# Optimization experiments

Measured on AMD Instinct MI355X. Metric: run time of the kernel, lower is better.

The kernel has to match this reference:

```python
import jax, jax.numpy as jnp
import numpy as np

# Static problem sizes (uniform T/taus make the ragged edge list static).
B, N, F, T, TAU, S = 8, 384, 64, 192, 192, 5
SINK_SHIFT = T                    # min sink index == T (sinks are the new nodes)
N_SINK, N_SOURCE = TAU, T + TAU - 1


def _edge_indices():
    # tril_indices(T+tau, offset=-1), keep sink >= T  (window=None)
    r, c = np.tril_indices(T + TAU, k=-1)
    m = r >= T
    r, c = r[m], c[m]
    e = r.shape[0]
    batch = np.repeat(np.arange(B), e)
    return (jnp.asarray(batch, jnp.int32),
            jnp.asarray(np.tile(r, B), jnp.int32),
            jnp.asarray(np.tile(c, B), jnp.int32))


def setup_inputs() -> dict:
    key = jax.random.key(0)
    ks = jax.random.split(key, 6)
    batch_idx, sink_idx, source_idx = _edge_indices()
    s1, s2 = 1.0 / np.sqrt(2 * F), 1.0 / np.sqrt(F)
    return {
        "nodes": jax.random.normal(ks[0], (B, N, F), jnp.float32),
        "w1": jax.random.uniform(ks[1], (2 * F, F), jnp.float32, -s1, s1),
        "b1": jnp.zeros((F,), jnp.float32),
        "g1": jnp.ones((F,), jnp.float32),
        "be1": jnp.zeros((F,), jnp.float32),
        "w2": jax.random.uniform(ks[2], (F, F), jnp.float32, -s2, s2),
        "b2": jnp.zeros((F,), jnp.float32),
        "g2": jnp.ones((F,), jnp.float32),
        "be2": jnp.zeros((F,), jnp.float32),
        "w3": jax.random.uniform(ks[3], (F, 1), jnp.float32, -s2, s2),
        "b3": jnp.zeros((1,), jnp.float32),
        "gumbel": jax.random.gumbel(ks[4], (S, B, N_SINK, N_SOURCE), jnp.float32),
        "batch_idx": batch_idx,
        "sink_idx": sink_idx,
        "source_idx": source_idx,
    }


def _ln(x, g, b):
    mu = x.mean(-1, keepdims=True)
    v = ((x - mu) ** 2).mean(-1, keepdims=True)
    return (x - mu) * jax.lax.rsqrt(v + 1e-5) * g + b


def reference(nodes, w1, b1, g1, be1, w2, b2, g2, be2, w3, b3,
              gumbel, batch_idx, sink_idx, source_idx):
    # gather sink/source node pairs: [E, 2F]
    sink = nodes[batch_idx, sink_idx]
    src = nodes[batch_idx, source_idx]
    x = jnp.concatenate([sink, src], axis=-1)
    # edge MLP -> per-edge logit
    h = _ln(jax.nn.relu(x @ w1 + b1), g1, be1)
    h = _ln(jax.nn.relu(h @ w2 + b2), g2, be2)
    logits = (h @ w3 + b3)[:, 0]                     # [E]
    # dense-padded grid filled with finfo.min (as in torch)
    neg = jnp.finfo(jnp.float32).min
    gs = jnp.full((B, N_SINK, N_SOURCE), neg, jnp.float32)
    gs = gs.at[batch_idx, sink_idx - SINK_SHIFT, source_idx].set(logits)
    # hard gumbel-softmax over source dim, S independent samples
    y_soft = jax.nn.softmax(gs[None] + gumbel, axis=-1)      # [S,B,192,383]
    y_hard = jax.nn.one_hot(jnp.argmax(y_soft, -1), N_SOURCE, dtype=y_soft.dtype)
    y = y_soft + jax.lax.stop_gradient(y_hard - y_soft)
    e = y.sum(0)
    # straight-through binarize: forward (e>0), backward identity
    e = e + jax.lax.stop_gradient((e > 0).astype(e.dtype) - e)
    valid = e[batch_idx, sink_idx - SINK_SHIFT, source_idx]
    vals = jnp.where(valid > 0, valid, 0.0)
    # dense equivalent of the sparse COO adjacency (B, N, N)
    return jnp.zeros((B, N, N), jnp.float32).at[batch_idx, sink_idx, source_idx].set(vals)
```

## Files before the change

kernel.cpp:

```cpp
#include <hip/hip_runtime.h>
#include <math.h>
#include <stdint.h>

#define BB 8
#define NN 384
#define FF 64
#define TT 192
#define NSRC 383
#define NSINK 192
#define SS 5
#define NEDGE 441600
#define BN (BB * NN)
#define TILE_E 256
#define NBLKE (NEDGE / TILE_E)
#define OUTV ((BB * NN * NN) / 4)

typedef _Float16 half8 __attribute__((ext_vector_type(8)));
typedef __fp16 fp16x2 __attribute__((ext_vector_type(2)));
typedef float floatx4 __attribute__((ext_vector_type(4)));

static __device__ __forceinline__ void split_f16(float x, uint16_t& h, uint16_t& l) {
  const _Float16 hh = (_Float16)x;
  const float hb = (float)hh;
  const _Float16 ll = (_Float16)((x - hb) * 512.f);
  h = __builtin_bit_cast(uint16_t, hh);
  l = __builtin_bit_cast(uint16_t, ll);
}

static __device__ __forceinline__ void split_pair(float x0, float x1,
                                                  uint32_t& hi, uint32_t& lo) {
  const fp16x2 h = __builtin_amdgcn_cvt_pkrtz(x0, x1);
  const float hb0 = (float)h.x, hb1 = (float)h.y;
  const fp16x2 l = __builtin_amdgcn_cvt_pkrtz((x0 - hb0) * 512.f, (x1 - hb1) * 512.f);
  hi = __builtin_bit_cast(uint32_t, h);
  lo = __builtin_bit_cast(uint32_t, l);
}

__global__ __launch_bounds__(64) void prep_all(
    const float* __restrict__ nodes, const float* __restrict__ w1,
    const float* __restrict__ b1,
    const float* __restrict__ w2, const float* __restrict__ b2,
    const float* __restrict__ g1, const float* __restrict__ be1,
    const float* __restrict__ g2, const float* __restrict__ be2,
    const float* __restrict__ w3, const float* __restrict__ b3,
    float* __restrict__ A, float* __restrict__ Bv,
    unsigned short* __restrict__ Whg, unsigned short* __restrict__ Wlg,
    float* __restrict__ wcol, float* __restrict__ cb,
    float* __restrict__ gw, float* __restrict__ cwsgw) {
  const int blk = blockIdx.x;
  const int k = threadIdx.x;
  if (blk < BN / 4) {
    const int bn0 = blk * 4;
    __shared__ float nd[4][FF];
#pragma unroll
    for (int i = 0; i < 4; ++i) nd[i][k] = nodes[(bn0 + i) * FF + k];
    __syncthreads();
    const float bk = b1[k];
    float a0 = bk, a1 = bk, a2 = bk, a3 = bk;
    float q0 = 0.f, q1 = 0.f, q2 = 0.f, q3 = 0.f;
#pragma unroll 8
    for (int f = 0; f < FF; ++f) {
      const float wt = w1[f * FF + k];
      const float wb = w1[(FF + f) * FF + k];
      const float n0 = nd[0][f], n1 = nd[1][f], n2 = nd[2][f], n3 = nd[3][f];
      a0 = fmaf(n0, wt, a0); a1 = fmaf(n1, wt, a1);
      a2 = fmaf(n2, wt, a2); a3 = fmaf(n3, wt, a3);
      q0 = fmaf(n0, wb, q0); q1 = fmaf(n1, wb, q1);
      q2 = fmaf(n2, wb, q2); q3 = fmaf(n3, wb, q3);
    }
    A[(bn0 + 0) * FF + k] = a0;  Bv[(bn0 + 0) * FF + k] = q0;
    A[(bn0 + 1) * FF + k] = a1;  Bv[(bn0 + 1) * FF + k] = q1;
    A[(bn0 + 2) * FF + k] = a2;  Bv[(bn0 + 2) * FF + k] = q2;
    A[(bn0 + 3) * FF + k] = a3;  Bv[(bn0 + 3) * FF + k] = q3;
  } else {
    const int j = k;
    const int jt = j >> 4, m = j & 15;
    float cbj = b2[j];
    float wc = 0.f;
    for (int kk = 0; kk < FF; ++kk) {
      const float wraw = w2[kk * FF + j];
      const float w = g1[kk] * wraw;
      wc += w;
      cbj = fmaf(be1[kk], wraw, cbj);
      uint16_t hu, lu;
      split_f16(w, hu, lu);
      const int kc = kk >> 5, qq = (kk >> 3) & 3, jj = kk & 7;
      const int idx = (((jt * 2 + kc) * 4 + qq) * 16 + m) * 8 + jj;
      Whg[idx] = hu;
      Wlg[idx] = lu;
    }
    wcol[j] = wc;
    cb[j] = cbj;
    const float gwj = g2[j] * w3[j];
    gw[j] = gwj;
    __shared__ float sA[FF], sB[FF];
    sA[j] = gwj;
    sB[j] = be2[j] * w3[j];
    __syncthreads();
    if (j == 0) {
      float a = 0.f, bq = 0.f;
      for (int i = 0; i < FF; ++i) { a += sA[i]; bq += sB[i]; }
      cwsgw[0] = b3[0] + bq;
      cwsgw[1] = a;
    }
  }
}

__global__ __launch_bounds__(256, 2) void edge_mlp(
    const float* __restrict__ A, const float* __restrict__ Bv,
    const unsigned short* __restrict__ Whg, const unsigned short* __restrict__ Wlg,
    const float* __restrict__ wcolg, const float* __restrict__ cbg,
    const float* __restrict__ gwg, const float* __restrict__ cwsgw,
    const int* __restrict__ bidx, const int* __restrict__ ridx,
    const int* __restrict__ cidx, float* __restrict__ L,
    float4* __restrict__ outv) {
  __shared__ __align__(16) unsigned short XHs[16384];
  __shared__ __align__(16) unsigned short XLs[16384];

  const int tid = threadIdx.x;
  const int wave = tid >> 6;
  const int lane = tid & 63;
  const int q4 = lane >> 4;
  const int c15 = lane & 15;

  const int gtid = blockIdx.x * 256 + tid;
  if (gtid < OUTV) outv[gtid] = make_float4(0.f, 0.f, 0.f, 0.f);

  half8 whr[4][2], wlr[4][2];
#pragma unroll
  for (int jt = 0; jt < 4; ++jt)
#pragma unroll
    for (int kc = 0; kc < 2; ++kc) {
      const int woff = ((jt * 2 + kc) * 4 + q4) * 128 + c15 * 8;
      whr[jt][kc] = *(const half8*)&Whg[woff];
      wlr[jt][kc] = *(const half8*)&Wlg[woff];
    }

  const int ge = blockIdx.x * TILE_E + tid;
  const int b = bidx[ge], r = ridx[ge], c = cidx[ge];
  const int et_own = lane >> 4, n_own = lane & 15;
  float mu, rstd;
  {
    const float4* pa = (const float4*)(A + (b * NN + r) * FF);
    const float4* pb = (const float4*)(Bv + (b * NN + c) * FF);
    unsigned short* dh = &XHs[wave * 4096 + n_own * 8];
    unsigned short* dl = &XLs[wave * 4096 + n_own * 8];
    float s = 0.f, q = 0.f;
#pragma unroll
    for (int g = 0; g < 8; ++g) {
      const float4 av0 = pa[2 * g], av1 = pa[2 * g + 1];
      const float4 bv0 = pb[2 * g], bv1 = pb[2 * g + 1];
      const float x0 = fmaxf(av0.x + bv0.x, 0.f);
      const float x1 = fmaxf(av0.y + bv0.y, 0.f);
      const float x2 = fmaxf(av0.z + bv0.z, 0.f);
      const float x3 = fmaxf(av0.w + bv0.w, 0.f);
      const float x4 = fmaxf(av1.x + bv1.x, 0.f);
      const float x5 = fmaxf(av1.y + bv1.y, 0.f);
      const float x6 = fmaxf(av1.z + bv1.z, 0.f);
      const float x7 = fmaxf(av1.w + bv1.w, 0.f);
      s += x0 + x1 + x2 + x3 + x4 + x5 + x6 + x7;
      q = fmaf(x0, x0, q); q = fmaf(x1, x1, q);
      q = fmaf(x2, x2, q); q = fmaf(x3, x3, q);
      q = fmaf(x4, x4, q); q = fmaf(x5, x5, q);
      q = fmaf(x6, x6, q); q = fmaf(x7, x7, q);
      int4 hi4, lo4;
      split_pair(x0, x1, *(uint32_t*)&hi4.x, *(uint32_t*)&lo4.x);
      split_pair(x2, x3, *(uint32_t*)&hi4.y, *(uint32_t*)&lo4.y);
      split_pair(x4, x5, *(uint32_t*)&hi4.z, *(uint32_t*)&lo4.z);
      split_pair(x6, x7, *(uint32_t*)&hi4.w, *(uint32_t*)&lo4.w);
      const int choff = ((et_own * 2 + (g >> 2)) * 4 + (g & 3)) * 128;
      *(int4*)(dh + choff) = hi4;
      *(int4*)(dl + choff) = lo4;
    }
    mu = s * (1.f / FF);
    rstd = 1.f / sqrtf(q * (1.f / FF) - mu * mu + 1e-5f);
  }

  __syncthreads();

  floatx4 wc4[4], cb4[4], gw4[4];
#pragma unroll
  for (int jt = 0; jt < 4; ++jt) {
    wc4[jt] = *(const floatx4*)(wcolg + 16 * jt + 4 * q4);
    cb4[jt] = *(const floatx4*)(cbg + 16 * jt + 4 * q4);
    gw4[jt] = *(const floatx4*)(gwg + 16 * jt + 4 * q4);
  }
  const float cw = cwsgw[0], sgw = cwsgw[1];

#pragma unroll
  for (int et = 0; et < 4; ++et) {
    floatx4 acc0[4], acc1[4];
#pragma unroll
    for (int jt = 0; jt < 4; ++jt) {
      acc0[jt] = (floatx4){0.f, 0.f, 0.f, 0.f};
      acc1[jt] = (floatx4){0.f, 0.f, 0.f, 0.f};
    }
#pragma unroll
    for (int kc = 0; kc < 2; ++kc) {
      const int xoff = wave * 4096 + ((et * 2 + kc) * 4 + q4) * 128 + c15 * 8;
      const half8 xh = *(const half8*)&XHs[xoff];
      const half8 xl = *(const half8*)&XLs[xoff];
#pragma unroll
      for (int jt = 0; jt < 4; ++jt) {
        acc0[jt] = __builtin_amdgcn_mfma_f32_16x16x32_f16(whr[jt][kc], xh, acc0[jt], 0, 0, 0);
        acc1[jt] = __builtin_amdgcn_mfma_f32_16x16x32_f16(whr[jt][kc], xl, acc1[jt], 0, 0, 0);
        acc1[jt] = __builtin_amdgcn_mfma_f32_16x16x32_f16(wlr[jt][kc], xh, acc1[jt], 0, 0, 0);
      }
    }
    const int e2 = 16 * et + c15;
    const float mue = __shfl(mu, e2, 64);
    const float rse = __shfl(rstd, e2, 64);
    float s1 = 0.f, s2 = 0.f, s3 = 0.f;
#pragma unroll
    for (int jt = 0; jt < 4; ++jt) {
      const floatx4 t4 = acc0[jt] + acc1[jt] * (1.f / 512.f);
#pragma unroll
      for (int rg = 0; rg < 4; ++rg) {
        const float pre = fmaf(rse, fmaf(-mue, wc4[jt][rg], t4[rg]), cb4[jt][rg]);
        const float tr = fmaxf(pre, 0.f);
        s1 += tr;
        s2 = fmaf(tr, tr, s2);
        s3 = fmaf(tr, gw4[jt][rg], s3);
      }
    }
    s1 += __shfl_xor(s1, 16, 64); s1 += __shfl_xor(s1, 32, 64);
    s2 += __shfl_xor(s2, 16, 64); s2 += __shfl_xor(s2, 32, 64);
    s3 += __shfl_xor(s3, 16, 64); s3 += __shfl_xor(s3, 32, 64);
    const int b2 = __shfl(b, e2, 64);
    const int r2 = __shfl(r, e2, 64);
    const int c2 = __shfl(c, e2, 64);
    if (q4 == 0) {
      const float mu2 = s1 * (1.f / FF);
      const float var2 = s2 * (1.f / FF) - mu2 * mu2;
      const float rstd2 = 1.f / sqrtf(var2 + 1e-5f);
      const float logit = fmaf(rstd2, fmaf(-mu2, sgw, s3), cw);
      L[(b2 * NSINK + (r2 - TT)) * NSRC + c2] = logit;
    }
  }
}

__global__ __launch_bounds__(256) void argmax_scatter(
    const float* __restrict__ L, const float* __restrict__ gum,
    float* __restrict__ out) {
  const int task = blockIdx.x * 4 + (threadIdx.x >> 6);
  const int lane = threadIdx.x & 63;
  const int row = task % NSINK;
  const int sb = task / NSINK;
  const int b = sb & 7;
  const int r = row + TT;

  const float* __restrict__ lrow = L + (b * NSINK + row) * NSRC;
  const float* __restrict__ grow = gum + task * NSRC;

  float bv = -INFINITY;
  int bi = 0;
  for (int c = lane; c < r; c += 64) {
    const float v = lrow[c] + grow[c];
    if (v > bv) { bv = v; bi = c; }
  }
#pragma unroll
  for (int off = 32; off > 0; off >>= 1) {
    const float ov = __shfl_xor(bv, off, 64);
    const int oi = __shfl_xor(bi, off, 64);
    if (ov > bv || (ov == bv && oi < bi)) { bv = ov; bi = oi; }
  }
  if (lane == 0) out[(b * NN + r) * NN + bi] = 1.0f;
}

extern "C" void kernel_launch(void* const* d_in, const int* in_sizes, int n_in,
                              void* d_out, int out_size, void* d_ws, size_t ws_size,
                              hipStream_t stream) {
  const float* nodes = (const float*)d_in[0];
  const float* w1 = (const float*)d_in[1];
  const float* b1 = (const float*)d_in[2];
  const float* g1 = (const float*)d_in[3];
  const float* be1 = (const float*)d_in[4];
  const float* w2 = (const float*)d_in[5];
  const float* b2 = (const float*)d_in[6];
  const float* g2 = (const float*)d_in[7];
  const float* be2 = (const float*)d_in[8];
  const float* w3 = (const float*)d_in[9];
  const float* b3 = (const float*)d_in[10];
  const float* gum = (const float*)d_in[11];
  const int* bidx = (const int*)d_in[12];
  const int* ridx = (const int*)d_in[13];
  const int* cidx = (const int*)d_in[14];
  float* out = (float*)d_out;

  float* ws = (float*)d_ws;
  float* A = ws;
  float* Bv = A + BN * FF;
  unsigned short* Whg = (unsigned short*)(ws + 393216);
  unsigned short* Wlg = Whg + 4096;
  float* wcol = ws + 397312;
  float* cb = wcol + FF;
  float* gw = cb + FF;
  float* cwsgw = gw + FF;
  float* L = ws + 397520;
  (void)ws_size; (void)n_in; (void)in_sizes; (void)out_size;

  hipLaunchKernelGGL(prep_all, dim3(BN / 4 + 1), dim3(64), 0, stream,
                     nodes, w1, b1, w2, b2, g1, be1, g2, be2, w3, b3,
                     A, Bv, Whg, Wlg, wcol, cb, gw, cwsgw);
  hipLaunchKernelGGL(edge_mlp, dim3(NBLKE), dim3(256), 0, stream,
                     A, Bv, Whg, Wlg, wcol, cb, gw, cwsgw, bidx, ridx, cidx, L,
                     (float4*)out);
  hipLaunchKernelGGL(argmax_scatter, dim3((SS * BB * NSINK) / 4), dim3(256), 0, stream,
                     L, gum, out);
}
```

Before: 132.9 us.

## Transpose B projection layout, defer weight loads, merge samples in argmax

The source-side projection Bv is stored feature-chunk-major, so adjacent edges (consecutive source columns) read adjacent float4s and the gather coalesces. The MFMA weight register loads move after the gather phase, and a __syncthreads is removed. argmax_scatter now handles all 5 gumbel samples in one wave per (batch,row), reading each logit once and cutting the wave count fivefold. The risks are less parallelism in argmax, higher register pressure, and a possible LDS race from the removed barrier if waves share XHs regions.

```diff
diff --git a/kernel.cpp b/kernel.cpp
--- a/kernel.cpp
+++ b/kernel.cpp
@@ -68,10 +68,15 @@
       q0 = fmaf(n0, wb, q0); q1 = fmaf(n1, wb, q1);
       q2 = fmaf(n2, wb, q2); q3 = fmaf(n3, wb, q3);
     }
-    A[(bn0 + 0) * FF + k] = a0;  Bv[(bn0 + 0) * FF + k] = q0;
-    A[(bn0 + 1) * FF + k] = a1;  Bv[(bn0 + 1) * FF + k] = q1;
-    A[(bn0 + 2) * FF + k] = a2;  Bv[(bn0 + 2) * FF + k] = q2;
-    A[(bn0 + 3) * FF + k] = a3;  Bv[(bn0 + 3) * FF + k] = q3;
+    A[(bn0 + 0) * FF + k] = a0;
+    A[(bn0 + 1) * FF + k] = a1;
+    A[(bn0 + 2) * FF + k] = a2;
+    A[(bn0 + 3) * FF + k] = a3;
+    const int f4 = k >> 2, ff = k & 3;
+    Bv[(f4 * BN + (bn0 + 0)) * 4 + ff] = q0;
+    Bv[(f4 * BN + (bn0 + 1)) * 4 + ff] = q1;
+    Bv[(f4 * BN + (bn0 + 2)) * 4 + ff] = q2;
+    Bv[(f4 * BN + (bn0 + 3)) * 4 + ff] = q3;
   } else {
     const int j = k;
     const int jt = j >> 4, m = j & 15;
@@ -126,30 +131,22 @@
   const int gtid = blockIdx.x * 256 + tid;
   if (gtid < OUTV) outv[gtid] = make_float4(0.f, 0.f, 0.f, 0.f);
 
-  half8 whr[4][2], wlr[4][2];
-#pragma unroll
-  for (int jt = 0; jt < 4; ++jt)
-#pragma unroll
-    for (int kc = 0; kc < 2; ++kc) {
-      const int woff = ((jt * 2 + kc) * 4 + q4) * 128 + c15 * 8;
-      whr[jt][kc] = *(const half8*)&Whg[woff];
-      wlr[jt][kc] = *(const half8*)&Wlg[woff];
-    }
-
   const int ge = blockIdx.x * TILE_E + tid;
   const int b = bidx[ge], r = ridx[ge], c = cidx[ge];
   const int et_own = lane >> 4, n_own = lane & 15;
   float mu, rstd;
   {
     const float4* pa = (const float4*)(A + (b * NN + r) * FF);
-    const float4* pb = (const float4*)(Bv + (b * NN + c) * FF);
+    const float4* pb4 = (const float4*)Bv;
+    const int colB = b * NN + c;
     unsigned short* dh = &XHs[wave * 4096 + n_own * 8];
     unsigned short* dl = &XLs[wave * 4096 + n_own * 8];
     float s = 0.f, q = 0.f;
 #pragma unroll
     for (int g = 0; g < 8; ++g) {
       const float4 av0 = pa[2 * g], av1 = pa[2 * g + 1];
-      const float4 bv0 = pb[2 * g], bv1 = pb[2 * g + 1];
+      const float4 bv0 = pb4[(2 * g) * BN + colB];
+      const float4 bv1 = pb4[(2 * g + 1) * BN + colB];
       const float x0 = fmaxf(av0.x + bv0.x, 0.f);
       const float x1 = fmaxf(av0.y + bv0.y, 0.f);
       const float x2 = fmaxf(av0.z + bv0.z, 0.f);
@@ -176,7 +173,15 @@
     rstd = 1.f / sqrtf(q * (1.f / FF) - mu * mu + 1e-5f);
   }
 
-  __syncthreads();
+  half8 whr[4][2], wlr[4][2];
+#pragma unroll
+  for (int jt = 0; jt < 4; ++jt)
+#pragma unroll
+    for (int kc = 0; kc < 2; ++kc) {
+      const int woff = ((jt * 2 + kc) * 4 + q4) * 128 + c15 * 8;
+      whr[jt][kc] = *(const half8*)&Whg[woff];
+      wlr[jt][kc] = *(const half8*)&Wlg[woff];
+    }
 
   floatx4 wc4[4], cb4[4], gw4[4];
 #pragma unroll
@@ -242,29 +247,62 @@
 __global__ __launch_bounds__(256) void argmax_scatter(
     const float* __restrict__ L, const float* __restrict__ gum,
     float* __restrict__ out) {
-  const int task = blockIdx.x * 4 + (threadIdx.x >> 6);
+  const int pair = blockIdx.x * 4 + (threadIdx.x >> 6);
   const int lane = threadIdx.x & 63;
-  const int row = task % NSINK;
-  const int sb = task / NSINK;
-  const int b = sb & 7;
+  const int row = pair % NSINK;
+  const int b = pair / NSINK;
   const int r = row + TT;
 
   const float* __restrict__ lrow = L + (b * NSINK + row) * NSRC;
-  const float* __restrict__ grow = gum + task * NSRC;
-
-  float bv = -INFINITY;
-  int bi = 0;
-  for (int c = lane; c < r; c += 64) {
-    const float v = lrow[c] + grow[c];
-    if (v > bv) { bv = v; bi = c; }
+  const float* __restrict__ g0 = gum + (b * NSINK + row) * NSRC;
+  const int sstr = BB * NSINK * NSRC;
+
+  float bv0 = -INFINITY, bv1 = -INFINITY, bv2 = -INFINITY, bv3 = -INFINITY, bv4 = -INFINITY;
+  int bi0 = 0, bi1 = 0, bi2 = 0, bi3 = 0, bi4 = 0;
+  for (int cc = lane; cc < r; cc += 64) {
+    const float lv = lrow[cc];
+    const float v0 = lv + g0[0 * sstr + cc];
+    const float v1 = lv + g0[1 * sstr + cc];
+    const float v2 = lv + g0[2 * sstr + cc];
+    const float v3 = lv + g0[3 * sstr + cc];
+    const float v4 = lv + g0[4 * sstr + cc];
+    if (v0 > bv0) { bv0 = v0; bi0 = cc; }
+    if (v1 > bv1) { bv1 = v1; bi1 = cc; }
+    if (v2 > bv2) { bv2 = v2; bi2 = cc; }
+    if (v3 > bv3) { bv3 = v3; bi3 = cc; }
+    if (v4 > bv4) { bv4 = v4; bi4 = cc; }
   }
 #pragma unroll
   for (int off = 32; off > 0; off >>= 1) {
-    const float ov = __shfl_xor(bv, off, 64);
-    const int oi = __shfl_xor(bi, off, 64);
-    if (ov > bv || (ov == bv && oi < bi)) { bv = ov; bi = oi; }
-  }
-  if (lane == 0) out[(b * NN + r) * NN + bi] = 1.0f;
+    {
+      const float ov = __shfl_xor(bv0, off, 64); const int oi = __shfl_xor(bi0, off, 64);
+      if (ov > bv0 || (ov == bv0 && oi < bi0)) { bv0 = ov; bi0 = oi; }
+    }
+    {
+      const float ov = __shfl_xor(bv1, off, 64); const int oi = __shfl_xor(bi1, off, 64);
+      if (ov > bv1 || (ov == bv1 && oi < bi1)) { bv1 = ov; bi1 = oi; }
+    }
+    {
+      const float ov = __shfl_xor(bv2, off, 64); const int oi = __shfl_xor(bi2, off, 64);
+      if (ov > bv2 || (ov == bv2 && oi < bi2)) { bv2 = ov; bi2 = oi; }
+    }
+    {
+      const float ov = __shfl_xor(bv3, off, 64); const int oi = __shfl_xor(bi3, off, 64);
+      if (ov > bv3 || (ov == bv3 && oi < bi3)) { bv3 = ov; bi3 = oi; }
+    }
+    {
+      const float ov = __shfl_xor(bv4, off, 64); const int oi = __shfl_xor(bi4, off, 64);
+      if (ov > bv4 || (ov == bv4 && oi < bi4)) { bv4 = ov; bi4 = oi; }
+    }
+  }
+  if (lane == 0) {
+    float* __restrict__ orow = out + (b * NN + r) * NN;
+    orow[bi0] = 1.0f;
+    orow[bi1] = 1.0f;
+    orow[bi2] = 1.0f;
+    orow[bi3] = 1.0f;
+    orow[bi4] = 1.0f;
+  }
 }
 
 extern "C" void kernel_launch(void* const* d_in, const int* in_sizes, int n_in,
@@ -305,6 +343,6 @@
   hipLaunchKernelGGL(edge_mlp, dim3(NBLKE), dim3(256), 0, stream,
                      A, Bv, Whg, Wlg, wcol, cb, gw, cwsgw, bidx, ridx, cidx, L,
                      (float4*)out);
-  hipLaunchKernelGGL(argmax_scatter, dim3((SS * BB * NSINK) / 4), dim3(256), 0, stream,
+  hipLaunchKernelGGL(argmax_scatter, dim3((BB * NSINK) / 4), dim3(256), 0, stream,
                      L, gum, out);
 }
```

New measurement: 129.6 us. -2.5%, faster.
